# Performance work log

Measured on AMD Instinct MI355X. Metric: run time of the kernel, lower is better.

## Reference

```python
import math
import jax, jax.numpy as jnp
import numpy as np

B, S, D, H = 2, 2048, 1024, 16
DH = D // H
EPS = 1e-5


def setup_inputs() -> dict:
    key = jax.random.key(0)
    ks = jax.random.split(key, 8)
    def lin(k, din, dout):
        return jax.random.normal(k, (din, dout), dtype=jnp.float32) / math.sqrt(din)
    return {
        "x": jax.random.normal(ks[0], (B, S, D), dtype=jnp.float32),
        "attention_mask": jnp.ones((B, S), dtype=jnp.int32),
        "Wq": lin(ks[1], D, D),
        "Wk": lin(ks[2], D, D),
        "Wv": lin(ks[3], D, D),
        "Wo": lin(ks[4], D, D),
        "W1": lin(ks[5], D, 4 * D),
        "W2": lin(ks[6], 2 * D, D),
        "gamma1": jnp.ones((D,), jnp.float32),
        "beta1": jnp.zeros((D,), jnp.float32),
        "gamma2": jnp.ones((D,), jnp.float32),
        "beta2": jnp.zeros((D,), jnp.float32),
    }


def layernorm(x, gamma, beta):
    mu = jnp.mean(x, axis=-1, keepdims=True)
    xc = x - mu
    var = jnp.mean(xc * xc, axis=-1, keepdims=True)
    return gamma * (xc / jnp.sqrt(var + EPS)) + beta


def softmax_last(x):
    x = x - jnp.max(x, axis=-1, keepdims=True)
    e = jnp.exp(x)
    return e / jnp.sum(e, axis=-1, keepdims=True)


def mhsa(x, attention_mask, Wq, Wk, Wv, Wo, causal=True):
    b, s, d = x.shape
    q = (x @ Wq).reshape(b, s, H, DH).transpose(0, 2, 1, 3)  # [b,h,s,dh]
    k = (x @ Wk).reshape(b, s, H, DH).transpose(0, 2, 1, 3)
    v = (x @ Wv).reshape(b, s, H, DH).transpose(0, 2, 1, 3)
    score = jnp.einsum("bhqd,bhkd->bhqk", q, k) / math.sqrt(DH)
    if causal:
        cmask = jnp.tril(jnp.ones((s, s), dtype=bool))
        score = jnp.where(cmask[None, None], score, -jnp.inf)
    key_mask = attention_mask.astype(bool)[:, None, None, :]  # [b,1,1,s]
    score = jnp.where(key_mask, score, -jnp.inf)
    attn = softmax_last(score)
    out = jnp.einsum("bhqk,bhkd->bhqd", attn, v)
    out = out.transpose(0, 2, 1, 3).reshape(b, s, d)
    return out @ Wo


def reference(x, attention_mask, Wq, Wk, Wv, Wo, W1, W2, gamma1, beta1, gamma2, beta2):
    x1 = x + mhsa(layernorm(x, gamma1, beta1), attention_mask, Wq, Wk, Wv, Wo, causal=True)
    h = layernorm(x1, gamma2, beta2) @ W1          # [b,s,4d]
    left, right = h[:, :, : 2 * D], h[:, :, 2 * D :]
    glu = left * jax.nn.sigmoid(right)             # [b,s,2d]
    return x1 + glu @ W2
```

## Files before the change

### kernel.cpp

```cpp
#include <hip/hip_runtime.h>
#include <hip/hip_bf16.h>
#include <math.h>

#define BB 2
#define SS 2048
#define DD 1024
#define HH 16
#define DH 64
#define NTOK (BB * SS)
#define LN_EPS 1e-5f
#define BIGNEG -1e30f

typedef __attribute__((ext_vector_type(8))) short bf16x8;
typedef __attribute__((ext_vector_type(4))) float f32x4;

static __device__ __forceinline__ unsigned short f2bu(float f) {
    __hip_bfloat16 h = __float2bfloat16(f);
    return *(unsigned short*)&h;
}

static __device__ __forceinline__ void async16(const void* g, void* l) {
    __builtin_amdgcn_global_load_lds((const __attribute__((address_space(1))) void*)g,
                                     (__attribute__((address_space(3))) void*)l, 16, 0, 0);
}


__global__ __launch_bounds__(256) void prep_kernel(const float* __restrict__ Wq,
                                                   const float* __restrict__ Wk,
                                                   const float* __restrict__ Wv,
                                                   const float* __restrict__ Wo,
                                                   const float* __restrict__ W1,
                                                   const float* __restrict__ W2,
                                                   __hip_bfloat16* __restrict__ wqkvt,
                                                   __hip_bfloat16* __restrict__ wot,
                                                   __hip_bfloat16* __restrict__ w1t,
                                                   __hip_bfloat16* __restrict__ w2t,
                                                   const float* __restrict__ x,
                                                   const float* __restrict__ gamma,
                                                   const float* __restrict__ beta,
                                                   __hip_bfloat16* __restrict__ lnb) {
    __shared__ float t[32][33];
    __shared__ float red[256];
    const int bid = blockIdx.x;
    const int tid = threadIdx.x;

    if (bid >= 10240) {
        const int row = bid - 10240;
        const float* xp = x + (size_t)row * DD;
        float vals[4];
        float s = 0.f;
#pragma unroll
        for (int i = 0; i < 4; ++i) {
            float v = xp[tid + i * 256];
            vals[i] = v;
            s += v;
        }
        red[tid] = s;
        __syncthreads();
        for (int st = 128; st > 0; st >>= 1) {
            if (tid < st) red[tid] += red[tid + st];
            __syncthreads();
        }
        const float mu = red[0] * (1.0f / DD);
        __syncthreads();
        float sq = 0.f;
#pragma unroll
        for (int i = 0; i < 4; ++i) {
            float d = vals[i] - mu;
            sq += d * d;
        }
        red[tid] = sq;
        __syncthreads();
        for (int st = 128; st > 0; st >>= 1) {
            if (tid < st) red[tid] += red[tid + st];
            __syncthreads();
        }
        const float rinv = rsqrtf(red[0] * (1.0f / DD) + LN_EPS);
        __hip_bfloat16* op = lnb + (size_t)row * DD;
#pragma unroll
        for (int i = 0; i < 4; ++i) {
            int j = tid + i * 256;
            op[j] = __float2bfloat16(gamma[j] * ((vals[i] - mu) * rinv) + beta[j]);
        }
        return;
    }

    const float* W;
    __hip_bfloat16* Wt;
    int K, N, tile;
    if (bid < 4096) {
        const int m = bid >> 10;
        tile = bid & 1023;
        W = (m == 0) ? Wq : (m == 1) ? Wk : (m == 2) ? Wv : Wo;
        Wt = (m < 3) ? (wqkvt + (size_t)m * 1024 * 1024) : wot;
        K = 1024; N = 1024;
    } else if (bid < 8192) {
        tile = bid - 4096; W = W1; Wt = w1t; K = 1024; N = 4096;
    } else {
        tile = bid - 8192; W = W2; Wt = w2t; K = 2048; N = 1024;
    }
    const int nt = N >> 5;
    const int n0 = (tile % nt) * 32, k0 = (tile / nt) * 32;
    const int tx = tid & 31, ty = tid >> 5;
#pragma unroll
    for (int i = 0; i < 4; ++i)
        t[ty + 8 * i][tx] = W[(size_t)(k0 + ty + 8 * i) * N + n0 + tx];
    __syncthreads();
#pragma unroll
    for (int i = 0; i < 4; ++i)
        Wt[(size_t)(n0 + ty + 8 * i) * K + k0 + tx] = __float2bfloat16(t[tx][ty + 8 * i]);
}

__global__ __launch_bounds__(256) void ln_kernel(const float* __restrict__ x,
                                                 const float* __restrict__ gamma,
                                                 const float* __restrict__ beta,
                                                 __hip_bfloat16* __restrict__ out) {
    const int row = blockIdx.x;
    const int tid = threadIdx.x;
    __shared__ float red[256];

    const float* xp = x + (size_t)row * DD;
    float vals[4];
    float s = 0.f;
#pragma unroll
    for (int i = 0; i < 4; ++i) {
        float v = xp[tid + i * 256];
        vals[i] = v;
        s += v;
    }
    red[tid] = s;
    __syncthreads();
    for (int st = 128; st > 0; st >>= 1) {
        if (tid < st) red[tid] += red[tid + st];
        __syncthreads();
    }
    const float mu = red[0] * (1.0f / DD);
    __syncthreads();
    float sq = 0.f;
#pragma unroll
    for (int i = 0; i < 4; ++i) {
        float d = vals[i] - mu;
        sq += d * d;
    }
    red[tid] = sq;
    __syncthreads();
    for (int st = 128; st > 0; st >>= 1) {
        if (tid < st) red[tid] += red[tid + st];
        __syncthreads();
    }
    const float rinv = rsqrtf(red[0] * (1.0f / DD) + LN_EPS);

    __hip_bfloat16* op = out + (size_t)row * DD;
#pragma unroll
    for (int i = 0; i < 4; ++i) {
        int j = tid + i * 256;
        op[j] = __float2bfloat16(gamma[j] * ((vals[i] - mu) * rinv) + beta[j]);
    }
}

template <int RES, int EPI>
__global__ __launch_bounds__(256) void mfma_gemm(const __hip_bfloat16* __restrict__ A,
                                                 const __hip_bfloat16* __restrict__ Bt,
                                                 const void* __restrict__ res,
                                                 void* __restrict__ out,
                                                 int M, int N, int K,
                                                 int xcdCols, int colGroups,
                                                 __hip_bfloat16* __restrict__ vtout) {
    __shared__ short As[128 * 64];
    __shared__ short Bs[128 * 64];
    const int tid = threadIdx.x;
    const int lane = tid & 63;
    const int wave = tid >> 6;
    const int xcd = blockIdx.x & 7;
    const int i = blockIdx.x >> 3;
    const int xcdRows = (gridDim.x >> 3) / xcdCols;
    const int r = i / xcdCols;
    const int c = i - r * xcdCols;
    const int rowg = xcd / colGroups;
    const int colg = xcd - rowg * colGroups;
    const int row0 = (rowg * xcdRows + r) * 128;
    const int col0 = (colg * xcdCols + c) * 128;
    const int wr = (wave >> 1) * 64;
    const int wc = (wave & 1) * 64;
    const int l15 = lane & 15;
    const int quad = lane >> 4;
    const int s7 = l15 & 7;

    f32x4 acc[4][4] = {};

    for (int k0 = 0; k0 < K; k0 += 64) {
#pragma unroll
        for (int rr = 0; rr < 4; ++rr) {
            const int ec = rr * 256 + tid;
            const int ar = ec >> 3, d = ec & 7;
            const int ao = (d ^ (ar & 7)) << 3;
            async16(&A[(size_t)(row0 + ar) * K + k0 + ao], &As[ec << 3]);
            async16(&Bt[(size_t)(col0 + ar) * K + k0 + ao], &Bs[ec << 3]);
        }
        __syncthreads();
#pragma unroll
        for (int kk = 0; kk < 2; ++kk) {
            const int co = (((kk << 2) | quad) ^ s7) << 3;
            bf16x8 af[4], bfr[4];
#pragma unroll
            for (int ii = 0; ii < 4; ++ii)
                af[ii] = *(const bf16x8*)&As[(wr + ii * 16 + l15) * 64 + co];
#pragma unroll
            for (int j = 0; j < 4; ++j)
                bfr[j] = *(const bf16x8*)&Bs[(wc + j * 16 + l15) * 64 + co];
#pragma unroll
            for (int ii = 0; ii < 4; ++ii)
#pragma unroll
                for (int j = 0; j < 4; ++j)
                    acc[ii][j] = __builtin_amdgcn_mfma_f32_16x16x32_bf16(af[ii], bfr[j], acc[ii][j], 0, 0, 0);
        }
        __syncthreads();
    }

    const int r4 = quad * 4;
    if (vtout != nullptr && col0 >= 2048) {
#pragma unroll
        for (int ii = 0; ii < 4; ++ii) {
#pragma unroll
            for (int j = 0; j < 4; ++j) {
                const int cc = col0 + wc + j * 16 + l15 - 2048;
                const int orow0 = row0 + wr + ii * 16 + r4;
                const unsigned long long pk =
                    (unsigned long long)(((unsigned)f2bu(acc[ii][j][3]) << 16) | f2bu(acc[ii][j][2])) << 32 |
                    (((unsigned)f2bu(acc[ii][j][1]) << 16) | f2bu(acc[ii][j][0]));
                *(unsigned long long*)((unsigned short*)vtout + (size_t)cc * 4096 + orow0) = pk;
            }
        }
        return;
    }
#pragma unroll
    for (int ii = 0; ii < 4; ++ii) {
#pragma unroll
        for (int j = 0; j < 4; ++j) {
            const int orow0 = row0 + wr + ii * 16 + r4;
            const int ocol = col0 + wc + j * 16 + l15;
#pragma unroll
            for (int rg = 0; rg < 4; ++rg) {
                const size_t oi = (size_t)(orow0 + rg) * N + ocol;
                float v = acc[ii][j][rg];
                if constexpr (RES == 1) v += ((const float*)res)[oi];
                if constexpr (EPI == 0) ((float*)out)[oi] = v;
                if constexpr (EPI == 1) ((__hip_bfloat16*)out)[oi] = __float2bfloat16(v);
            }
        }
    }
}

template <int RES, int EPI>
__global__ __launch_bounds__(256) void mfma_gemm_n64(const __hip_bfloat16* __restrict__ A,
                                                     const __hip_bfloat16* __restrict__ Bt,
                                                     const void* __restrict__ res,
                                                     void* __restrict__ out,
                                                     int N, int K, int colTiles) {
    __shared__ short As[128 * 64];
    __shared__ short Bs[64 * 64];
    const int tid = threadIdx.x;
    const int lane = tid & 63;
    const int wave = tid >> 6;
    const int cpx = gridDim.x >> 3;
    const int wg = (blockIdx.x & 7) * cpx + (blockIdx.x >> 3);
    const int row0 = (wg / colTiles) * 128;
    const int col0 = (wg % colTiles) * 64;
    const int wr = wave * 32;
    const int l15 = lane & 15;
    const int quad = lane >> 4;
    const int s7 = l15 & 7;

    f32x4 acc[2][4] = {};

    for (int k0 = 0; k0 < K; k0 += 64) {
#pragma unroll
        for (int r = 0; r < 4; ++r) {
            const int ec = r * 256 + tid;
            const int ar = ec >> 3, d = ec & 7;
            const int ao = (d ^ (ar & 7)) << 3;
            async16(&A[(size_t)(row0 + ar) * K + k0 + ao], &As[ec << 3]);
        }
#pragma unroll
        for (int r = 0; r < 2; ++r) {
            const int ec = r * 256 + tid;
            const int ar = ec >> 3, d = ec & 7;
            const int ao = (d ^ (ar & 7)) << 3;
            async16(&Bt[(size_t)(col0 + ar) * K + k0 + ao], &Bs[ec << 3]);
        }
        __syncthreads();
#pragma unroll
        for (int kk = 0; kk < 2; ++kk) {
            const int co = (((kk << 2) | quad) ^ s7) << 3;
            bf16x8 af[2], bfr[4];
#pragma unroll
            for (int i = 0; i < 2; ++i)
                af[i] = *(const bf16x8*)&As[(wr + i * 16 + l15) * 64 + co];
#pragma unroll
            for (int j = 0; j < 4; ++j)
                bfr[j] = *(const bf16x8*)&Bs[(j * 16 + l15) * 64 + co];
#pragma unroll
            for (int i = 0; i < 2; ++i)
#pragma unroll
                for (int j = 0; j < 4; ++j)
                    acc[i][j] = __builtin_amdgcn_mfma_f32_16x16x32_bf16(af[i], bfr[j], acc[i][j], 0, 0, 0);
        }
        __syncthreads();
    }

    const int r4 = quad * 4;
#pragma unroll
    for (int i = 0; i < 2; ++i) {
#pragma unroll
        for (int j = 0; j < 4; ++j) {
            const int orow0 = row0 + wr + i * 16 + r4;
            const int ocol = col0 + j * 16 + l15;
#pragma unroll
            for (int rg = 0; rg < 4; ++rg) {
                const size_t oi = (size_t)(orow0 + rg) * N + ocol;
                float v = acc[i][j][rg];
                if constexpr (RES == 1) v += ((const float*)res)[oi];
                if constexpr (EPI == 0) ((float*)out)[oi] = v;
                if constexpr (EPI == 1) ((__hip_bfloat16*)out)[oi] = __float2bfloat16(v);
            }
        }
    }
}

__global__ __launch_bounds__(256) void mfma_gemm_glu64(const __hip_bfloat16* __restrict__ A,
                                                       const __hip_bfloat16* __restrict__ Bt,
                                                       __hip_bfloat16* __restrict__ out) {
    __shared__ short As[128 * 64];
    __shared__ short Bl[64 * 64];
    __shared__ short Br[64 * 64];
    const int tid = threadIdx.x;
    const int lane = tid & 63;
    const int wave = tid >> 6;
    const int xcd = blockIdx.x & 7;
    const int i = blockIdx.x >> 3;
    const int row0 = ((xcd >> 1) * 8 + (i >> 4)) * 128;
    const int col0 = ((xcd & 1) * 16 + (i & 15)) * 64;
    const int wr = wave * 32;
    const int l15 = lane & 15;
    const int quad = lane >> 4;
    const int s7 = l15 & 7;

    f32x4 accl[2][4] = {};
    f32x4 accr[2][4] = {};

    for (int k0 = 0; k0 < 1024; k0 += 64) {
#pragma unroll
        for (int r = 0; r < 4; ++r) {
            const int ec = r * 256 + tid;
            const int ar = ec >> 3, d = ec & 7;
            const int ao = (d ^ (ar & 7)) << 3;
            async16(&A[(size_t)(row0 + ar) * 1024 + k0 + ao], &As[ec << 3]);
        }
#pragma unroll
        for (int r = 0; r < 2; ++r) {
            const int ec = r * 256 + tid;
            const int ar = ec >> 3, d = ec & 7;
            const int ao = (d ^ (ar & 7)) << 3;
            async16(&Bt[(size_t)(col0 + ar) * 1024 + k0 + ao], &Bl[ec << 3]);
            async16(&Bt[(size_t)(2048 + col0 + ar) * 1024 + k0 + ao], &Br[ec << 3]);
        }
        __syncthreads();
#pragma unroll
        for (int kk = 0; kk < 2; ++kk) {
            const int co = (((kk << 2) | quad) ^ s7) << 3;
            bf16x8 af[2], bl[4], br[4];
#pragma unroll
            for (int ii = 0; ii < 2; ++ii)
                af[ii] = *(const bf16x8*)&As[(wr + ii * 16 + l15) * 64 + co];
#pragma unroll
            for (int j = 0; j < 4; ++j) {
                bl[j] = *(const bf16x8*)&Bl[(j * 16 + l15) * 64 + co];
                br[j] = *(const bf16x8*)&Br[(j * 16 + l15) * 64 + co];
            }
#pragma unroll
            for (int ii = 0; ii < 2; ++ii)
#pragma unroll
                for (int j = 0; j < 4; ++j) {
                    accl[ii][j] = __builtin_amdgcn_mfma_f32_16x16x32_bf16(af[ii], bl[j], accl[ii][j], 0, 0, 0);
                    accr[ii][j] = __builtin_amdgcn_mfma_f32_16x16x32_bf16(af[ii], br[j], accr[ii][j], 0, 0, 0);
                }
        }
        __syncthreads();
    }

    const int r4 = quad * 4;
#pragma unroll
    for (int ii = 0; ii < 2; ++ii) {
#pragma unroll
        for (int j = 0; j < 4; ++j) {
#pragma unroll
            for (int rg = 0; rg < 4; ++rg) {
                const int orow = row0 + wr + ii * 16 + r4 + rg;
                const int ocol = col0 + j * 16 + l15;
                const float l = accl[ii][j][rg];
                const float r = accr[ii][j][rg];
                out[(size_t)orow * 2048 + ocol] =
                    __float2bfloat16(l * (1.f / (1.f + __expf(-r))));
            }
        }
    }
}

#define KADV (64 * 3072)
#define RESCALE_THR 8.f

__global__ __launch_bounds__(256, 4) void flash_mfma(const __hip_bfloat16* __restrict__ qkv_,
                                                     const __hip_bfloat16* __restrict__ VT_,
                                                     const int* __restrict__ mask,
                                                     __hip_bfloat16* __restrict__ attnb) {
    const unsigned short* qkv = (const unsigned short*)qkv_;
    const unsigned short* VT = (const unsigned short*)VT_;
    __shared__ __align__(16) short Ks[2][64 * 64];
    __shared__ __align__(16) short Vt[2][64 * 64];
    __shared__ __align__(16) short Ps[4][16 * 64];

    const int tid = threadIdx.x;
    const int lane = tid & 63;
    const int wave = tid >> 6;
    const int l15 = lane & 15;
    const int quad = lane >> 4;
    const int s7 = l15 & 7;

    const int xcd = blockIdx.x & 7;
    const int slot = blockIdx.x >> 3;
    const int bh = xcd + ((slot & 3) << 3);
    const int v = slot >> 2;
    const int vr = v & 7, vs = v >> 3;
    const int qt = (vs == 0) ? 31 - vr : (vs == 1) ? vr : (vs == 2) ? 23 - vr : 8 + vr;
    const int h = bh & 15;
    const int b = bh >> 4;
    const int q0 = qt * 64 + wave * 16;

    const int e0 = tid, e1 = 256 + tid;
    const int r0 = e0 >> 3, d0 = e0 & 7, r1 = e1 >> 3, d1 = e1 & 7;
    const unsigned short* kp0 = qkv + (size_t)(b * SS + r0) * 3072 + 1024 + h * 64 + ((d0 ^ (r0 & 7)) << 3);
    const unsigned short* kp1 = qkv + (size_t)(b * SS + r1) * 3072 + 1024 + h * 64 + ((d1 ^ (r1 & 7)) << 3);
    const unsigned short* vp0 = VT + (size_t)(h * 64 + r0) * 4096 + b * SS + ((d0 ^ (r0 & 7)) << 3);
    const unsigned short* vp1 = VT + (size_t)(h * 64 + r1) * 4096 + b * SS + ((d1 ^ (r1 & 7)) << 3);
    short* const kd0a = &Ks[0][e0 << 3]; short* const kd0b = &Ks[1][e0 << 3];
    short* const kd1a = &Ks[0][e1 << 3]; short* const kd1b = &Ks[1][e1 << 3];
    short* const vd0a = &Vt[0][e0 << 3]; short* const vd0b = &Vt[1][e0 << 3];
    short* const vd1a = &Vt[0][e1 << 3]; short* const vd1b = &Vt[1][e1 << 3];

    const int* const mrow = mask + b * SS;

    bf16x8 aq[2];
#pragma unroll
    for (int ks = 0; ks < 2; ++ks)
        aq[ks] = *(const bf16x8*)(qkv + (size_t)(b * SS + q0 + l15) * 3072 +
                                  h * 64 + ks * 32 + quad * 8);

    f32x4 O[4];
#pragma unroll
    for (int i = 0; i < 4; ++i) O[i] = (f32x4){0.f, 0.f, 0.f, 0.f};
    float m_r = BIGNEG, l_r = 0.f;

    short* const Pw = &Ps[wave][0];

    async16(kp0, kd0a); async16(kp1, kd1a);
    async16(vp0, vd0a); async16(vp1, vd1a);
    kp0 += KADV; kp1 += KADV; vp0 += 64; vp1 += 64;

    for (int c = 0; c < qt; ++c) {
        const int cur = c & 1;
        __syncthreads();

        async16(kp0, cur ? kd0a : kd0b);
        async16(kp1, cur ? kd1a : kd1b);
        async16(vp0, cur ? vd0a : vd0b);
        async16(vp1, cur ? vd1a : vd1b);
        kp0 += KADV; kp1 += KADV; vp0 += 64; vp1 += 64;

        const int kb = c << 6;
        const short* Kc = &Ks[cur][0];
        const short* Vc = &Vt[cur][0];

        int4 mv[4];
#pragma unroll
        for (int kt = 0; kt < 4; ++kt)
            mv[kt] = *(const int4*)&mrow[kb + kt * 16 + quad * 4];

        f32x4 S[4];
        __builtin_amdgcn_s_setprio(1);
#pragma unroll
        for (int kt = 0; kt < 4; ++kt) {
            const bf16x8 bk0 = *(const bf16x8*)&Kc[(kt * 16 + l15) * 64 + ((quad ^ s7) << 3)];
            const bf16x8 bk1 = *(const bf16x8*)&Kc[(kt * 16 + l15) * 64 + (((4 | quad) ^ s7) << 3)];
            f32x4 z = {0.f, 0.f, 0.f, 0.f};
            z = __builtin_amdgcn_mfma_f32_16x16x32_bf16(bk0, aq[0], z, 0, 0, 0);
            S[kt] = __builtin_amdgcn_mfma_f32_16x16x32_bf16(bk1, aq[1], z, 0, 0, 0);
        }
        __builtin_amdgcn_s_setprio(0);

#pragma unroll
        for (int kt = 0; kt < 4; ++kt) {
            const int* mm = (const int*)&mv[kt];
#pragma unroll
            for (int rg = 0; rg < 4; ++rg)
                S[kt][rg] = fmaf(S[kt][rg], 0.125f, mm[rg] ? 0.f : BIGNEG);
        }

        const float t0 = fmaxf(fmaxf(S[0][0], S[0][1]), fmaxf(S[0][2], S[0][3]));
        const float t1 = fmaxf(fmaxf(S[1][0], S[1][1]), fmaxf(S[1][2], S[1][3]));
        const float t2 = fmaxf(fmaxf(S[2][0], S[2][1]), fmaxf(S[2][2], S[2][3]));
        const float t3 = fmaxf(fmaxf(S[3][0], S[3][1]), fmaxf(S[3][2], S[3][3]));
        float tmax = fmaxf(fmaxf(t0, t1), fmaxf(t2, t3));
        tmax = fmaxf(tmax, __shfl_xor(tmax, 16));
        tmax = fmaxf(tmax, __shfl_xor(tmax, 32));

        if (__any(tmax > m_r + RESCALE_THR)) {
            const float mn = fmaxf(m_r, tmax);
            const float alpha = __expf(m_r - mn);
            m_r = mn;
            l_r *= alpha;
#pragma unroll
            for (int nt = 0; nt < 4; ++nt)
#pragma unroll
                for (int rg = 0; rg < 4; ++rg)
                    O[nt][rg] *= alpha;
        }

        float rsum = 0.f;
        unsigned long long p64[4];
#pragma unroll
        for (int kt = 0; kt < 4; ++kt) {
#pragma unroll
            for (int rg = 0; rg < 4; ++rg)
                S[kt][rg] = __expf(S[kt][rg] - m_r);
            rsum += (S[kt][0] + S[kt][1]) + (S[kt][2] + S[kt][3]);
            p64[kt] = ((unsigned long long)(((unsigned)f2bu(S[kt][3]) << 16) | f2bu(S[kt][2])) << 32)
                    | (((unsigned)f2bu(S[kt][1]) << 16) | f2bu(S[kt][0]));
        }
        rsum += __shfl_xor(rsum, 16);
        rsum += __shfl_xor(rsum, 32);
        l_r += rsum;

#pragma unroll
        for (int kt = 0; kt < 4; ++kt) {
            const int ch = (kt << 1) | (quad >> 1);
            const int base = (l15 << 6) + ((ch ^ s7) << 3) + ((quad & 1) << 2);
            *(unsigned long long*)&Pw[base] = p64[kt];
        }

        __builtin_amdgcn_s_setprio(1);
#pragma unroll
        for (int kk = 0; kk < 2; ++kk) {
            const int co = ((((kk << 2) | quad) ^ s7) << 3);
            const bf16x8 bp = *(const bf16x8*)&Pw[(l15 << 6) + co];
#pragma unroll
            for (int nt = 0; nt < 4; ++nt) {
                const bf16x8 av = *(const bf16x8*)&Vc[(nt * 16 + l15) * 64 + co];
                O[nt] = __builtin_amdgcn_mfma_f32_16x16x32_bf16(av, bp, O[nt], 0, 0, 0);
            }
        }
        __builtin_amdgcn_s_setprio(0);
    }

    {
        const int cur = qt & 1;
        __syncthreads();

        const int kb = qt << 6;
        const int ktmax = wave + 1;
        const int ktfull = wave;
        const short* Kc = &Ks[cur][0];
        const short* Vc = &Vt[cur][0];
        const int qrow = q0 + l15;

        int4 mv[4];
#pragma unroll
        for (int kt = 0; kt < 4; ++kt) {
            if (kt >= ktmax) break;
            mv[kt] = *(const int4*)&mrow[kb + kt * 16 + quad * 4];
        }

        f32x4 S[4];
        __builtin_amdgcn_s_setprio(1);
#pragma unroll
        for (int kt = 0; kt < 4; ++kt) {
            if (kt >= ktmax) break;
            const bf16x8 bk0 = *(const bf16x8*)&Kc[(kt * 16 + l15) * 64 + ((quad ^ s7) << 3)];
            const bf16x8 bk1 = *(const bf16x8*)&Kc[(kt * 16 + l15) * 64 + (((4 | quad) ^ s7) << 3)];
            f32x4 z = {0.f, 0.f, 0.f, 0.f};
            z = __builtin_amdgcn_mfma_f32_16x16x32_bf16(bk0, aq[0], z, 0, 0, 0);
            S[kt] = __builtin_amdgcn_mfma_f32_16x16x32_bf16(bk1, aq[1], z, 0, 0, 0);
        }
        __builtin_amdgcn_s_setprio(0);

#pragma unroll
        for (int kt = 0; kt < 4; ++kt) {
            if (kt >= ktmax) break;
            const int* mm = (const int*)&mv[kt];
#pragma unroll
            for (int rg = 0; rg < 4; ++rg) {
                float s = fmaf(S[kt][rg], 0.125f, mm[rg] ? 0.f : BIGNEG);
                if (kt >= ktfull) {
                    const int key = kb + kt * 16 + quad * 4 + rg;
                    s = (key <= qrow) ? s : BIGNEG;
                }
                S[kt][rg] = s;
            }
        }

        float tmax = BIGNEG;
#pragma unroll
        for (int kt = 0; kt < 4; ++kt) {
            if (kt >= ktmax) break;
            tmax = fmaxf(tmax, fmaxf(fmaxf(S[kt][0], S[kt][1]),
                                     fmaxf(S[kt][2], S[kt][3])));
        }
        tmax = fmaxf(tmax, __shfl_xor(tmax, 16));
        tmax = fmaxf(tmax, __shfl_xor(tmax, 32));

        if (__any(tmax > m_r + RESCALE_THR)) {
            const float mn = fmaxf(m_r, tmax);
            const float alpha = __expf(m_r - mn);
            m_r = mn;
            l_r *= alpha;
#pragma unroll
            for (int nt = 0; nt < 4; ++nt)
#pragma unroll
                for (int rg = 0; rg < 4; ++rg)
                    O[nt][rg] *= alpha;
        }

        float rsum = 0.f;
#pragma unroll
        for (int kt = 0; kt < 4; ++kt) {
            if (kt >= ktmax) break;
#pragma unroll
            for (int rg = 0; rg < 4; ++rg)
                S[kt][rg] = __expf(S[kt][rg] - m_r);
            rsum += (S[kt][0] + S[kt][1]) + (S[kt][2] + S[kt][3]);
            const int ch = (kt << 1) | (quad >> 1);
            const int base = (l15 << 6) + ((ch ^ s7) << 3) + ((quad & 1) << 2);
            *(unsigned long long*)&Pw[base] =
                ((unsigned long long)(((unsigned)f2bu(S[kt][3]) << 16) | f2bu(S[kt][2])) << 32)
                | (((unsigned)f2bu(S[kt][1]) << 16) | f2bu(S[kt][0]));
        }
        rsum += __shfl_xor(rsum, 16);
        rsum += __shfl_xor(rsum, 32);
        l_r += rsum;

        const int kkmax = (ktmax + 1) >> 1;
        if (ktmax & 1) {
            const int ch = (ktmax << 1) | (quad >> 1);
            const int base = (l15 << 6) + ((ch ^ s7) << 3) + ((quad & 1) << 2);
            *(unsigned long long*)&Pw[base] = 0ull;
        }

        __builtin_amdgcn_s_setprio(1);
#pragma unroll
        for (int kk = 0; kk < 2; ++kk) {
            if (kk >= kkmax) break;
            const int co = ((((kk << 2) | quad) ^ s7) << 3);
            const bf16x8 bp = *(const bf16x8*)&Pw[(l15 << 6) + co];
#pragma unroll
            for (int nt = 0; nt < 4; ++nt) {
                const bf16x8 av = *(const bf16x8*)&Vc[(nt * 16 + l15) * 64 + co];
                O[nt] = __builtin_amdgcn_mfma_f32_16x16x32_bf16(av, bp, O[nt], 0, 0, 0);
            }
        }
        __builtin_amdgcn_s_setprio(0);
    }

    const float inv = 1.f / l_r;
    unsigned short* op = (unsigned short*)attnb +
                         (size_t)(b * SS + q0 + l15) * 1024 + h * 64 + quad * 4;
#pragma unroll
    for (int nt = 0; nt < 4; ++nt) {
        const float o0 = O[nt][0] * inv, o1 = O[nt][1] * inv;
        const float o2 = O[nt][2] * inv, o3 = O[nt][3] * inv;
        const unsigned long long pk =
            (unsigned long long)(((unsigned)f2bu(o3) << 16) | f2bu(o2)) << 32 |
            (((unsigned)f2bu(o1) << 16) | f2bu(o0));
        *(unsigned long long*)(op + nt * 16) = pk;
    }
}

extern "C" void kernel_launch(void* const* d_in, const int* in_sizes, int n_in,
                              void* d_out, int out_size, void* d_ws, size_t ws_size,
                              hipStream_t stream) {
    const float* x  = (const float*)d_in[0];
    const int* mask = (const int*)d_in[1];
    const float* Wq = (const float*)d_in[2];
    const float* Wk = (const float*)d_in[3];
    const float* Wv = (const float*)d_in[4];
    const float* Wo = (const float*)d_in[5];
    const float* W1 = (const float*)d_in[6];
    const float* W2 = (const float*)d_in[7];
    const float* g1 = (const float*)d_in[8];
    const float* b1 = (const float*)d_in[9];
    const float* g2 = (const float*)d_in[10];
    const float* b2 = (const float*)d_in[11];

    const size_t MB = 1024 * 1024;
    uint8_t* ws = (uint8_t*)d_ws;
    __hip_bfloat16* wqkvt = (__hip_bfloat16*)(ws);
    __hip_bfloat16* wot   = (__hip_bfloat16*)(ws + 6 * MB);
    __hip_bfloat16* w1t   = (__hip_bfloat16*)(ws + 8 * MB);
    __hip_bfloat16* w2t   = (__hip_bfloat16*)(ws + 16 * MB);
    __hip_bfloat16* lnb   = (__hip_bfloat16*)(ws + 20 * MB);
    __hip_bfloat16* qkvb  = (__hip_bfloat16*)(ws + 28 * MB);
    float*          x1    = (float*)(ws + 28 * MB);
    __hip_bfloat16* attnb = (__hip_bfloat16*)(ws + 52 * MB);
    __hip_bfloat16* VT    = (__hip_bfloat16*)(ws + 60 * MB);
    __hip_bfloat16* glub  = (__hip_bfloat16*)(ws + 68 * MB);

    prep_kernel<<<10240 + NTOK, 256, 0, stream>>>(Wq, Wk, Wv, Wo, W1, W2,
                                                  wqkvt, wot, w1t, w2t,
                                                  x, g1, b1, lnb);

    mfma_gemm<0, 1><<<768, 256, 0, stream>>>(lnb, wqkvt, nullptr, qkvb,
                                             NTOK, 3072, 1024, 12, 2, VT);

    flash_mfma<<<1024, 256, 0, stream>>>(qkvb, VT, mask, attnb);

    mfma_gemm_n64<1, 0><<<512, 256, 0, stream>>>(attnb, wot, x, x1, 1024, 1024, 16);

    ln_kernel<<<NTOK, 256, 0, stream>>>(x1, g2, b2, lnb);

    mfma_gemm_glu64<<<1024, 256, 0, stream>>>(lnb, w1t, glub);

    mfma_gemm_n64<1, 0><<<512, 256, 0, stream>>>(glub, w2t, x1, (float*)d_out,
                                                 1024, 2048, 16);
}
```

Before: 192.4 us.

## Keep P in registers via 16x16x16 MFMA, compute row sums with ones-MFMA, use exp2

The flash attention kernel no longer stages the probability tile through shared memory. The S accumulator layout is fed directly as the B operand of 16x16x16 bf16 MFMAs, and V is read in 4-element slices. Row sums are now computed by an extra MFMA against a ones vector instead of shuffle reductions. The softmax uses exp2 with log2e folded into the scale. This removes LDS writes and reads and the cross-lane shuffles, in exchange for twice as many smaller MFMA instructions plus extra ones-MFMAs, and row sums built from bf16-rounded probabilities.

```diff
diff --git a/kernel.cpp b/kernel.cpp
--- a/kernel.cpp
+++ b/kernel.cpp
@@ -12,11 +12,16 @@
 #define BIGNEG -1e30f
 
 typedef __attribute__((ext_vector_type(8))) short bf16x8;
+typedef __attribute__((ext_vector_type(4))) short bf16x4;
 typedef __attribute__((ext_vector_type(4))) float f32x4;
 
 static __device__ __forceinline__ unsigned short f2bu(float f) {
     __hip_bfloat16 h = __float2bfloat16(f);
     return *(unsigned short*)&h;
+}
+
+static __device__ __forceinline__ f32x4 mfma16(bf16x4 a, bf16x4 b, f32x4 c) {
+    return __builtin_amdgcn_mfma_f32_16x16x16bf16_1k(a, b, c, 0, 0, 0);
 }
 
 static __device__ __forceinline__ void async16(const void* g, void* l) {
@@ -407,7 +412,8 @@
 }
 
 #define KADV (64 * 3072)
-#define RESCALE_THR 8.f
+#define SCL2E 0.1803368801f
+#define RESCALE_THR2 11.5f
 
 __global__ __launch_bounds__(256, 4) void flash_mfma(const __hip_bfloat16* __restrict__ qkv_,
                                                      const __hip_bfloat16* __restrict__ VT_,
@@ -417,7 +423,6 @@
     const unsigned short* VT = (const unsigned short*)VT_;
     __shared__ __align__(16) short Ks[2][64 * 64];
     __shared__ __align__(16) short Vt[2][64 * 64];
-    __shared__ __align__(16) short Ps[4][16 * 64];
 
     const int tid = threadIdx.x;
     const int lane = tid & 63;
@@ -455,12 +460,13 @@
         aq[ks] = *(const bf16x8*)(qkv + (size_t)(b * SS + q0 + l15) * 3072 +
                                   h * 64 + ks * 32 + quad * 8);
 
+    const bf16x4 onesA = {(short)0x3F80, (short)0x3F80, (short)0x3F80, (short)0x3F80};
+
     f32x4 O[4];
 #pragma unroll
     for (int i = 0; i < 4; ++i) O[i] = (f32x4){0.f, 0.f, 0.f, 0.f};
-    float m_r = BIGNEG, l_r = 0.f;
-
-    short* const Pw = &Ps[wave][0];
+    f32x4 accL = (f32x4){0.f, 0.f, 0.f, 0.f};
+    float m_r = BIGNEG;
 
     async16(kp0, kd0a); async16(kp1, kd1a);
     async16(vp0, vd0a); async16(vp1, vd1a);
@@ -502,7 +508,7 @@
             const int* mm = (const int*)&mv[kt];
 #pragma unroll
             for (int rg = 0; rg < 4; ++rg)
-                S[kt][rg] = fmaf(S[kt][rg], 0.125f, mm[rg] ? 0.f : BIGNEG);
+                S[kt][rg] = fmaf(S[kt][rg], SCL2E, mm[rg] ? 0.f : BIGNEG);
         }
 
         const float t0 = fmaxf(fmaxf(S[0][0], S[0][1]), fmaxf(S[0][2], S[0][3]));
@@ -513,11 +519,11 @@
         tmax = fmaxf(tmax, __shfl_xor(tmax, 16));
         tmax = fmaxf(tmax, __shfl_xor(tmax, 32));
 
-        if (__any(tmax > m_r + RESCALE_THR)) {
+        if (__any(tmax > m_r + RESCALE_THR2)) {
             const float mn = fmaxf(m_r, tmax);
-            const float alpha = __expf(m_r - mn);
+            const float alpha = exp2f(m_r - mn);
             m_r = mn;
-            l_r *= alpha;
+            accL *= alpha;
 #pragma unroll
             for (int nt = 0; nt < 4; ++nt)
 #pragma unroll
@@ -525,37 +531,27 @@
                     O[nt][rg] *= alpha;
         }
 
-        float rsum = 0.f;
         unsigned long long p64[4];
 #pragma unroll
         for (int kt = 0; kt < 4; ++kt) {
 #pragma unroll
             for (int rg = 0; rg < 4; ++rg)
-                S[kt][rg] = __expf(S[kt][rg] - m_r);
-            rsum += (S[kt][0] + S[kt][1]) + (S[kt][2] + S[kt][3]);
+                S[kt][rg] = exp2f(S[kt][rg] - m_r);
             p64[kt] = ((unsigned long long)(((unsigned)f2bu(S[kt][3]) << 16) | f2bu(S[kt][2])) << 32)
                     | (((unsigned)f2bu(S[kt][1]) << 16) | f2bu(S[kt][0]));
         }
-        rsum += __shfl_xor(rsum, 16);
-        rsum += __shfl_xor(rsum, 32);
-        l_r += rsum;
-
-#pragma unroll
-        for (int kt = 0; kt < 4; ++kt) {
-            const int ch = (kt << 1) | (quad >> 1);
-            const int base = (l15 << 6) + ((ch ^ s7) << 3) + ((quad & 1) << 2);
-            *(unsigned long long*)&Pw[base] = p64[kt];
-        }
 
         __builtin_amdgcn_s_setprio(1);
 #pragma unroll
-        for (int kk = 0; kk < 2; ++kk) {
-            const int co = ((((kk << 2) | quad) ^ s7) << 3);
-            const bf16x8 bp = *(const bf16x8*)&Pw[(l15 << 6) + co];
+        for (int kt = 0; kt < 4; ++kt) {
+            union { unsigned long long u; bf16x4 v; } pu; pu.u = p64[kt];
+            const bf16x4 bp = pu.v;
+            accL = mfma16(onesA, bp, accL);
+            const int vo = ((((kt << 1) | (quad >> 1)) ^ s7) << 3) + ((quad & 1) << 2);
 #pragma unroll
             for (int nt = 0; nt < 4; ++nt) {
-                const bf16x8 av = *(const bf16x8*)&Vc[(nt * 16 + l15) * 64 + co];
-                O[nt] = __builtin_amdgcn_mfma_f32_16x16x32_bf16(av, bp, O[nt], 0, 0, 0);
+                const bf16x4 av = *(const bf16x4*)&Vc[(nt * 16 + l15) * 64 + vo];
+                O[nt] = mfma16(av, bp, O[nt]);
             }
         }
         __builtin_amdgcn_s_setprio(0);
@@ -598,7 +594,7 @@
             const int* mm = (const int*)&mv[kt];
 #pragma unroll
             for (int rg = 0; rg < 4; ++rg) {
-                float s = fmaf(S[kt][rg], 0.125f, mm[rg] ? 0.f : BIGNEG);
+                float s = fmaf(S[kt][rg], SCL2E, mm[rg] ? 0.f : BIGNEG);
                 if (kt >= ktfull) {
                     const int key = kb + kt * 16 + quad * 4 + rg;
                     s = (key <= qrow) ? s : BIGNEG;
@@ -617,11 +613,11 @@
         tmax = fmaxf(tmax, __shfl_xor(tmax, 16));
         tmax = fmaxf(tmax, __shfl_xor(tmax, 32));
 
-        if (__any(tmax > m_r + RESCALE_THR)) {
+        if (__any(tmax > m_r + RESCALE_THR2)) {
             const float mn = fmaxf(m_r, tmax);
-            const float alpha = __expf(m_r - mn);
+            const float alpha = exp2f(m_r - mn);
             m_r = mn;
-            l_r *= alpha;
+            accL *= alpha;
 #pragma unroll
             for (int nt = 0; nt < 4; ++nt)
 #pragma unroll
@@ -629,47 +625,29 @@
                     O[nt][rg] *= alpha;
         }
 
-        float rsum = 0.f;
+        __builtin_amdgcn_s_setprio(1);
 #pragma unroll
         for (int kt = 0; kt < 4; ++kt) {
             if (kt >= ktmax) break;
 #pragma unroll
             for (int rg = 0; rg < 4; ++rg)
-                S[kt][rg] = __expf(S[kt][rg] - m_r);
-            rsum += (S[kt][0] + S[kt][1]) + (S[kt][2] + S[kt][3]);
-            const int ch = (kt << 1) | (quad >> 1);
-            const int base = (l15 << 6) + ((ch ^ s7) << 3) + ((quad & 1) << 2);
-            *(unsigned long long*)&Pw[base] =
-                ((unsigned long long)(((unsigned)f2bu(S[kt][3]) << 16) | f2bu(S[kt][2])) << 32)
-                | (((unsigned)f2bu(S[kt][1]) << 16) | f2bu(S[kt][0]));
-        }
-        rsum += __shfl_xor(rsum, 16);
-        rsum += __shfl_xor(rsum, 32);
-        l_r += rsum;
-
-        const int kkmax = (ktmax + 1) >> 1;
-        if (ktmax & 1) {
-            const int ch = (ktmax << 1) | (quad >> 1);
-            const int base = (l15 << 6) + ((ch ^ s7) << 3) + ((quad & 1) << 2);
-            *(unsigned long long*)&Pw[base] = 0ull;
-        }
-
-        __builtin_amdgcn_s_setprio(1);
-#pragma unroll
-        for (int kk = 0; kk < 2; ++kk) {
-            if (kk >= kkmax) break;
-            const int co = ((((kk << 2) | quad) ^ s7) << 3);
-            const bf16x8 bp = *(const bf16x8*)&Pw[(l15 << 6) + co];
+                S[kt][rg] = exp2f(S[kt][rg] - m_r);
+            union { unsigned long long u; bf16x4 v; } pu;
+            pu.u = ((unsigned long long)(((unsigned)f2bu(S[kt][3]) << 16) | f2bu(S[kt][2])) << 32)
+                 | (((unsigned)f2bu(S[kt][1]) << 16) | f2bu(S[kt][0]));
+            const bf16x4 bp = pu.v;
+            accL = mfma16(onesA, bp, accL);
+            const int vo = ((((kt << 1) | (quad >> 1)) ^ s7) << 3) + ((quad & 1) << 2);
 #pragma unroll
             for (int nt = 0; nt < 4; ++nt) {
-                const bf16x8 av = *(const bf16x8*)&Vc[(nt * 16 + l15) * 64 + co];
-                O[nt] = __builtin_amdgcn_mfma_f32_16x16x32_bf16(av, bp, O[nt], 0, 0, 0);
+                const bf16x4 av = *(const bf16x4*)&Vc[(nt * 16 + l15) * 64 + vo];
+                O[nt] = mfma16(av, bp, O[nt]);
             }
         }
         __builtin_amdgcn_s_setprio(0);
     }
 
-    const float inv = 1.f / l_r;
+    const float inv = 1.f / accL[0];
     unsigned short* op = (unsigned short*)attnb +
                          (size_t)(b * SS + q0 + l15) * 1024 + h * 64 + quad * 4;
 #pragma unroll
```

New measurement: 197.1 us. 1.02x slower.
